# Kernel optimization log

Hardware: AMD Instinct MI355X
Metric: run time of the kernel (lower is better)

Reference implementation:

```python
import jax, jax.numpy as jnp
import numpy as np

B, T, C, H = 4096, 32, 180, 6
HD = C // H  # 30
EPS = 1e-5

def _ln(x, g, b):
    mu = jnp.mean(x, axis=-1, keepdims=True)
    var = jnp.mean(jnp.square(x - mu), axis=-1, keepdims=True)
    return (x - mu) * jax.lax.rsqrt(var + EPS) * g + b

def setup_inputs() -> dict:
    key = jax.random.key(0)
    ks = jax.random.split(key, 12)
    s_in = 1.0 / np.sqrt(C)
    s_ff = 1.0 / np.sqrt(4 * C)
    return {
        "x": jax.random.normal(ks[0], (B, T, C), jnp.float32),
        "wq": jax.random.normal(ks[1], (H, C, HD), jnp.float32) * s_in,
        "wk": jax.random.normal(ks[2], (H, C, HD), jnp.float32) * s_in,
        "wv": jax.random.normal(ks[3], (H, C, HD), jnp.float32) * s_in,
        "g1": jnp.ones((C,), jnp.float32),
        "be1": jnp.zeros((C,), jnp.float32),
        "g2": jnp.ones((C,), jnp.float32),
        "be2": jnp.zeros((C,), jnp.float32),
        "w1": jax.random.normal(ks[4], (C, 4 * C), jnp.float32) * s_in,
        "b1": jnp.zeros((4 * C,), jnp.float32),
        "w2": jax.random.normal(ks[5], (4 * C, C), jnp.float32) * s_ff,
        "b2": jnp.zeros((C,), jnp.float32),
    }

def reference(x, wq, wk, wv, g1, be1, g2, be2, w1, b1, w2, b2):
    Bv, Tv, Cv = x.shape
    h = _ln(x, g1, be1)
    # batched multi-head QKV (replaces per-head Python loop)
    q = jnp.einsum('btc,hcd->bhtd', h, wq)
    k = jnp.einsum('btc,hcd->bhtd', h, wk)
    v = jnp.einsum('btc,hcd->bhtd', h, wv)
    scores = jnp.einsum('bhtd,bhsd->bhts', q, k) * (HD ** -0.5)
    mask = jnp.tril(jnp.ones((Tv, Tv), bool))
    scores = jnp.where(mask, scores, -jnp.inf)
    attn = jax.nn.softmax(scores, axis=-1)  # dropout off (eval)
    out = jnp.einsum('bhts,bhsd->bhtd', attn, v)
    out = jnp.transpose(out, (0, 2, 1, 3)).reshape(Bv, Tv, Cv)  # concat heads
    x = x + out
    h2 = _ln(x, g2, be2)
    mlp = jax.nn.relu(h2 @ w1 + b1) @ w2 + b2  # dropout off (eval)
    return x + mlp
```

## Files before the change

### kernel.cpp

```cpp
#include <hip/hip_runtime.h>

typedef __attribute__((ext_vector_type(8))) short short8;
typedef __attribute__((ext_vector_type(4))) float f32x4;
typedef __attribute__((ext_vector_type(2))) float f32x2;
typedef unsigned short ushort_t;
typedef unsigned int u32;
typedef unsigned long long u64;

#define MFMA16(a,b,c) __builtin_amdgcn_mfma_f32_16x16x32_bf16((a),(b),(c),0,0,0)

__device__ __forceinline__ ushort_t f2bf(float f){
  union { float f; u32 u; } v; v.f = f;
  u32 r = v.u + 0x7fffu + ((v.u >> 16) & 1u);
  return (ushort_t)(r >> 16);
}
__device__ __forceinline__ float bf2f(ushort_t h){
  union { u32 u; float f; } v; v.u = ((u32)h) << 16; return v.f;
}
__device__ __forceinline__ u64 pack4(float a, float b, float c, float d){
  u32 p0 = (u32)f2bf(a) | ((u32)f2bf(b) << 16);
  u32 p1 = (u32)f2bf(c) | ((u32)f2bf(d) << 16);
  return (u64)p0 | ((u64)p1 << 32);
}

template<int CTRL>
__device__ __forceinline__ float dpp_add(float x){
  union { float f; int i; } a, b;
  a.f = x;
  b.i = __builtin_amdgcn_update_dpp(a.i, a.i, CTRL, 0xF, 0xF, false);
  return x + b.f;
}
__device__ __forceinline__ float red4_add(float x){
  x = dpp_add<0xB1>(x); x = dpp_add<0x4E>(x);
  return x;
}

#define WQKV_ELEMS (576*192)
#define W1T_ELEMS  (768*192)
#define W2T_ELEMS  (192*768)

#define SH 200
#define SS 40

__global__ void prep_weights(const float* __restrict__ wq, const float* __restrict__ wk,
                             const float* __restrict__ wv, const float* __restrict__ w1,
                             const float* __restrict__ w2, ushort_t* __restrict__ ws){
  ushort_t* wqkv = ws;
  ushort_t* w1t = ws + WQKV_ELEMS;
  ushort_t* w2t = w1t + W1T_ELEMS;
  int tid = blockIdx.x * blockDim.x + threadIdx.x;
  int stride = gridDim.x * blockDim.x;
  for (int i = tid; i < WQKV_ELEMS; i += stride){
    int k = i % 192; int row = i / 192;
    int d = row & 31; int m = (row >> 5) % 3; int h = row / 96;
    float v = 0.f;
    if (d < 30 && k < 180){
      const float* W = (m == 0) ? wq : ((m == 1) ? wk : wv);
      v = W[(h*180 + k)*30 + d];
    }
    wqkv[i] = f2bf(v);
  }
  for (int i = tid; i < W1T_ELEMS; i += stride){
    int c = i % 192; int n = i / 192;
    float v = (n < 720 && c < 180) ? w1[c*720 + n] : 0.f;
    w1t[i] = f2bf(v);
  }
  for (int i = tid; i < W2T_ELEMS; i += stride){
    int c4 = i % 768; int n = i / 768;
    float v = (n < 180 && c4 < 720) ? w2[c4*180 + n] : 0.f;
    w2t[i] = f2bf(v);
  }
}

__device__ __forceinline__ void ln_pass(const ushort_t* src, ushort_t* dst,
                                        const float* __restrict__ g,
                                        const float* __restrict__ be, int tid){
  int row = tid >> 2, sub = tid & 3;
  int c0 = sub*48;
  float s1 = 0.f, s2 = 0.f;
  #pragma unroll
  for (int gi = 0; gi < 12; gi++){
    u64 m = *(const u64*)(src + row*SH + c0 + gi*4);
    #pragma unroll
    for (int e = 0; e < 4; e++){
      float v = bf2f((ushort_t)(m >> (16*e)));
      s1 += v; s2 += v*v;
    }
  }
  s1 = red4_add(s1); s2 = red4_add(s2);
  float mu = s1 * (1.f/180.f);
  float rstd = rsqrtf(s2 * (1.f/180.f) - mu*mu + 1e-5f);
  #pragma unroll
  for (int gi = 0; gi < 12; gi++){
    int c = c0 + gi*4;
    if (c < 180){
      u64 m = *(const u64*)(src + row*SH + c);
      f32x4 gg = *(const f32x4*)(g + c);
      f32x4 bb = *(const f32x4*)(be + c);
      float v0 = (bf2f((ushort_t)(m    )) - mu)*rstd*gg.x + bb.x;
      float v1 = (bf2f((ushort_t)(m>>16)) - mu)*rstd*gg.y + bb.y;
      float v2 = (bf2f((ushort_t)(m>>32)) - mu)*rstd*gg.z + bb.z;
      float v3 = (bf2f((ushort_t)(m>>48)) - mu)*rstd*gg.w + bb.w;
      *(u64*)(dst + row*SH + c) = pack4(v0, v1, v2, v3);
    } else {
      *(u64*)(dst + row*SH + c) = 0ull;
    }
  }
}

__global__ __launch_bounds__(256, 3)
void block_kernel(const float* __restrict__ x,
                  const float* __restrict__ g1, const float* __restrict__ be1,
                  const float* __restrict__ g2, const float* __restrict__ be2,
                  const float* __restrict__ b1, const float* __restrict__ b2,
                  const ushort_t* __restrict__ wqkv, const ushort_t* __restrict__ w1t,
                  const ushort_t* __restrict__ w2t, float* __restrict__ out){
  __shared__ __align__(16) ushort_t regA[64*SH];
  __shared__ __align__(16) ushort_t hn[64*SH];

  int tid = threadIdx.x;
  int wave = tid >> 6, lane = tid & 63;
  int quad = lane >> 4, c16 = lane & 15;
  long base = (long)blockIdx.x * 11520;

  #pragma unroll
  for (int it = 0; it < 12; it++){
    int idx = it*256 + tid;
    if (idx < 2880){
      f32x4 v = *(const f32x4*)(x + base + (long)idx*4);
      int row = (int)(((u32)idx * 745655u) >> 25);
      int col = idx - row*45;
      *(u64*)(regA + row*SH + col*4) = pack4(v.x, v.y, v.z, v.w);
    } else {
      int p = idx - 2880;
      int row = (p*21846) >> 16;
      int g = p - row*3;
      *(u64*)(regA + row*SH + 180 + g*4) = 0ull;
    }
  }
  __syncthreads();

  ln_pass(regA, hn, g1, be1, tid);
  __syncthreads();

  {
    ushort_t* buf0 = regA + wave*(2*32*SS);
    ushort_t* buf1 = buf0 + 32*SS;
    const float scl = 0.18257418583505537f;

    for (int jj = 0; jj < 3; jj++){
      int j = wave*3 + jj;
      int bb = (j >= 6) ? 1 : 0;
      int head = j - 6*bb;
      const ushort_t* wbase = wqkv + head*(96*192);

      f32x4 accq[2][2], acck[2][2], accv[2][2];
      #pragma unroll
      for (int i = 0; i < 2; i++)
        #pragma unroll
        for (int jx = 0; jx < 2; jx++){ accq[i][jx]=(f32x4)0.f; acck[i][jx]=(f32x4)0.f; accv[i][jx]=(f32x4)0.f; }

      short8 aqc[2], akc[2], avc[2];
      #pragma unroll
      for (int mt = 0; mt < 2; mt++){
        aqc[mt] = *(const short8*)(wbase + (      mt*16 + c16)*192 + quad*8);
        akc[mt] = *(const short8*)(wbase + (32  + mt*16 + c16)*192 + quad*8);
        avc[mt] = *(const short8*)(wbase + (64  + mt*16 + c16)*192 + quad*8);
      }
      #pragma unroll
      for (int kk = 0; kk < 6; kk++){
        short8 aqn[2], akn[2], avn[2];
        if (kk < 5){
          #pragma unroll
          for (int mt = 0; mt < 2; mt++){
            aqn[mt] = *(const short8*)(wbase + (      mt*16 + c16)*192 + (kk+1)*32 + quad*8);
            akn[mt] = *(const short8*)(wbase + (32  + mt*16 + c16)*192 + (kk+1)*32 + quad*8);
            avn[mt] = *(const short8*)(wbase + (64  + mt*16 + c16)*192 + (kk+1)*32 + quad*8);
          }
        }
        short8 hf[2];
        #pragma unroll
        for (int nt = 0; nt < 2; nt++)
          hf[nt] = *(const short8*)(hn + (bb*32 + nt*16 + c16)*SH + kk*32 + quad*8);
        #pragma unroll
        for (int mt = 0; mt < 2; mt++)
          #pragma unroll
          for (int nt = 0; nt < 2; nt++){
            accq[mt][nt] = MFMA16(aqc[mt], hf[nt], accq[mt][nt]);
            acck[mt][nt] = MFMA16(akc[mt], hf[nt], acck[mt][nt]);
            accv[mt][nt] = MFMA16(hf[mt], avc[nt], accv[mt][nt]);
          }
        if (kk < 5){
          #pragma unroll
          for (int mt = 0; mt < 2; mt++){ aqc[mt]=aqn[mt]; akc[mt]=akn[mt]; avc[mt]=avn[mt]; }
        }
      }
      #pragma unroll
      for (int mt = 0; mt < 2; mt++)
        #pragma unroll
        for (int nt = 0; nt < 2; nt++){
          *(u64*)(buf0 + (nt*16 + c16)*SS + mt*16 + quad*4) =
            pack4(accq[mt][nt][0], accq[mt][nt][1], accq[mt][nt][2], accq[mt][nt][3]);
          *(u64*)(buf1 + (nt*16 + c16)*SS + mt*16 + quad*4) =
            pack4(acck[mt][nt][0], acck[mt][nt][1], acck[mt][nt][2], acck[mt][nt][3]);
        }
      f32x4 sacc[2][2];
      #pragma unroll
      for (int i = 0; i < 2; i++){ sacc[i][0]=(f32x4)0.f; sacc[i][1]=(f32x4)0.f; }
      short8 akf[2], bqf[2];
      #pragma unroll
      for (int mt = 0; mt < 2; mt++) akf[mt] = *(const short8*)(buf1 + (mt*16 + c16)*SS + quad*8);
      #pragma unroll
      for (int nt = 0; nt < 2; nt++) bqf[nt] = *(const short8*)(buf0 + (nt*16 + c16)*SS + quad*8);
      #pragma unroll
      for (int mt = 0; mt < 2; mt++)
        #pragma unroll
        for (int nt = 0; nt < 2; nt++)
          sacc[mt][nt] = MFMA16(akf[mt], bqf[nt], sacc[mt][nt]);
      #pragma unroll
      for (int nt = 0; nt < 2; nt++){
        int t = nt*16 + c16;
        float v[8];
        #pragma unroll
        for (int r = 0; r < 4; r++){
          int s0 = quad*4 + r, s1v = 16 + quad*4 + r;
          v[r]   = (s0  > t) ? -1e30f : sacc[0][nt][r]*scl;
          v[4+r] = (s1v > t) ? -1e30f : sacc[1][nt][r]*scl;
        }
        float m = v[0];
        #pragma unroll
        for (int i = 1; i < 8; i++) m = fmaxf(m, v[i]);
        m = fmaxf(m, __shfl_xor(m, 16));
        m = fmaxf(m, __shfl_xor(m, 32));
        float e[8], s = 0.f;
        #pragma unroll
        for (int i = 0; i < 8; i++){ e[i] = __expf(v[i] - m); s += e[i]; }
        s += __shfl_xor(s, 16);
        s += __shfl_xor(s, 32);
        float inv = 1.f / s;
        *(u64*)(buf1 + t*SS +      quad*4) = pack4(e[0]*inv, e[1]*inv, e[2]*inv, e[3]*inv);
        *(u64*)(buf1 + t*SS + 16 + quad*4) = pack4(e[4]*inv, e[5]*inv, e[6]*inv, e[7]*inv);
      }
      #pragma unroll
      for (int mt = 0; mt < 2; mt++)
        #pragma unroll
        for (int nt = 0; nt < 2; nt++)
          *(u64*)(buf0 + (nt*16 + c16)*SS + mt*16 + quad*4) =
            pack4(accv[mt][nt][0], accv[mt][nt][1], accv[mt][nt][2], accv[mt][nt][3]);
      f32x4 oacc[2][2];
      #pragma unroll
      for (int i = 0; i < 2; i++){ oacc[i][0]=(f32x4)0.f; oacc[i][1]=(f32x4)0.f; }
      short8 avf[2], bpf[2];
      #pragma unroll
      for (int mt = 0; mt < 2; mt++) avf[mt] = *(const short8*)(buf0 + (mt*16 + c16)*SS + quad*8);
      #pragma unroll
      for (int nt = 0; nt < 2; nt++) bpf[nt] = *(const short8*)(buf1 + (nt*16 + c16)*SS + quad*8);
      #pragma unroll
      for (int mt = 0; mt < 2; mt++)
        #pragma unroll
        for (int nt = 0; nt < 2; nt++)
          oacc[mt][nt] = MFMA16(avf[mt], bpf[nt], oacc[mt][nt]);
      #pragma unroll
      for (int mt = 0; mt < 2; mt++)
        #pragma unroll
        for (int nt = 0; nt < 2; nt++){
          long ob = base + (long)(bb*32 + nt*16 + c16)*180 + head*30 + mt*16 + quad*4;
          f32x2 lo; lo.x = oacc[mt][nt][0]; lo.y = oacc[mt][nt][1];
          *(f32x2*)(out + ob) = lo;
          if (mt == 0 || quad < 3){
            f32x2 hi; hi.x = oacc[mt][nt][2]; hi.y = oacc[mt][nt][3];
            *(f32x2*)(out + ob + 2) = hi;
          }
        }
    }
  }
  __syncthreads();

  #pragma unroll
  for (int it = 0; it < 12; it++){
    int idx = it*256 + tid;
    if (idx < 2880){
      f32x4 v = *(const f32x4*)(x + base + (long)idx*4);
      f32x4 a = *(const f32x4*)(out + base + (long)idx*4);
      int row = (int)(((u32)idx * 745655u) >> 25);
      int col = idx - row*45;
      *(u64*)(regA + row*SH + col*4) = pack4(v.x+a.x, v.y+a.y, v.z+a.z, v.w+a.w);
    } else {
      int p = idx - 2880;
      int row = (p*21846) >> 16;
      int g = p - row*3;
      *(u64*)(regA + row*SH + 180 + g*4) = 0ull;
    }
  }
  __syncthreads();

  ln_pass(regA, hn, g2, be2, tid);
  __syncthreads();

  {
    ushort_t* act = regA;
    f32x4 outacc[3][4];
    #pragma unroll
    for (int i = 0; i < 3; i++)
      #pragma unroll
      for (int jx = 0; jx < 4; jx++) outacc[i][jx] = (f32x4)0.f;

    for (int ch = 0; ch < 4; ch++){
      f32x4 aacc[3][4];
      #pragma unroll
      for (int i = 0; i < 3; i++)
        #pragma unroll
        for (int jx = 0; jx < 4; jx++) aacc[i][jx] = (f32x4)0.f;
      short8 awc[3];
      #pragma unroll
      for (int mi = 0; mi < 3; mi++)
        awc[mi] = *(const short8*)(w1t + (size_t)(ch*192 + (wave*3+mi)*16 + c16)*192 + quad*8);
      #pragma unroll
      for (int kk = 0; kk < 6; kk++){
        short8 awn[3];
        if (kk < 5){
          #pragma unroll
          for (int mi = 0; mi < 3; mi++)
            awn[mi] = *(const short8*)(w1t + (size_t)(ch*192 + (wave*3+mi)*16 + c16)*192 + (kk+1)*32 + quad*8);
        }
        short8 bh[4];
        #pragma unroll
        for (int tt = 0; tt < 4; tt++)
          bh[tt] = *(const short8*)(hn + (tt*16 + c16)*SH + kk*32 + quad*8);
        #pragma unroll
        for (int mi = 0; mi < 3; mi++)
          #pragma unroll
          for (int tt = 0; tt < 4; tt++)
            aacc[mi][tt] = MFMA16(awc[mi], bh[tt], aacc[mi][tt]);
        if (kk < 5){
          #pragma unroll
          for (int mi = 0; mi < 3; mi++) awc[mi] = awn[mi];
        }
      }
      __syncthreads();
      #pragma unroll
      for (int mi = 0; mi < 3; mi++){
        int nrel = (wave*3+mi)*16 + quad*4;
        int nabs = ch*192 + nrel;
        f32x4 bias = (f32x4)0.f;
        if (nabs < 720) bias = *(const f32x4*)(b1 + nabs);
        #pragma unroll
        for (int tt = 0; tt < 4; tt++){
          float v0 = fmaxf(aacc[mi][tt][0] + bias[0], 0.f);
          float v1 = fmaxf(aacc[mi][tt][1] + bias[1], 0.f);
          float v2 = fmaxf(aacc[mi][tt][2] + bias[2], 0.f);
          float v3 = fmaxf(aacc[mi][tt][3] + bias[3], 0.f);
          *(u64*)(act + (tt*16 + c16)*SH + nrel) = pack4(v0, v1, v2, v3);
        }
      }
      __syncthreads();
      short8 bwc[3];
      #pragma unroll
      for (int ntl = 0; ntl < 3; ntl++)
        bwc[ntl] = *(const short8*)(w2t + (size_t)(wave*48 + ntl*16 + c16)*768 + ch*192 + quad*8);
      #pragma unroll
      for (int kk = 0; kk < 6; kk++){
        short8 bwn[3];
        if (kk < 5){
          #pragma unroll
          for (int ntl = 0; ntl < 3; ntl++)
            bwn[ntl] = *(const short8*)(w2t + (size_t)(wave*48 + ntl*16 + c16)*768 + ch*192 + (kk+1)*32 + quad*8);
        }
        short8 aa[4];
        #pragma unroll
        for (int tt = 0; tt < 4; tt++)
          aa[tt] = *(const short8*)(act + (tt*16 + c16)*SH + kk*32 + quad*8);
        #pragma unroll
        for (int ntl = 0; ntl < 3; ntl++)
          #pragma unroll
          for (int tt = 0; tt < 4; tt++)
            outacc[ntl][tt] = MFMA16(bwc[ntl], aa[tt], outacc[ntl][tt]);
        if (kk < 5){
          #pragma unroll
          for (int ntl = 0; ntl < 3; ntl++) bwc[ntl] = bwn[ntl];
        }
      }
    }
    #pragma unroll
    for (int ntl = 0; ntl < 3; ntl++){
      int no = wave*48 + ntl*16 + quad*4;
      #pragma unroll
      for (int tt = 0; tt < 4; tt++)
        *(u64*)(hn + (tt*16 + c16)*SH + no) =
          pack4(outacc[ntl][tt][0], outacc[ntl][tt][1], outacc[ntl][tt][2], outacc[ntl][tt][3]);
    }
  }
  __syncthreads();

  #pragma unroll
  for (int it = 0; it < 12; it++){
    int idx = it*256 + tid;
    if (idx < 2880){
      f32x4 v = *(const f32x4*)(x + base + (long)idx*4);
      f32x4 a = *(const f32x4*)(out + base + (long)idx*4);
      int row = (int)(((u32)idx * 745655u) >> 25);
      int col4 = (idx - row*45)*4;
      f32x4 b2v = *(const f32x4*)(b2 + col4);
      u64 m = *(const u64*)(hn + row*SH + col4);
      v.x += a.x + bf2f((ushort_t)(m      )) + b2v.x;
      v.y += a.y + bf2f((ushort_t)(m >> 16)) + b2v.y;
      v.z += a.z + bf2f((ushort_t)(m >> 32)) + b2v.z;
      v.w += a.w + bf2f((ushort_t)(m >> 48)) + b2v.w;
      *(f32x4*)(out + base + (long)idx*4) = v;
    }
  }
}

extern "C" void kernel_launch(void* const* d_in, const int* in_sizes, int n_in,
                              void* d_out, int out_size, void* d_ws, size_t ws_size,
                              hipStream_t stream) {
  const float* x   = (const float*)d_in[0];
  const float* wq  = (const float*)d_in[1];
  const float* wk  = (const float*)d_in[2];
  const float* wv  = (const float*)d_in[3];
  const float* g1  = (const float*)d_in[4];
  const float* be1 = (const float*)d_in[5];
  const float* g2  = (const float*)d_in[6];
  const float* be2 = (const float*)d_in[7];
  const float* w1  = (const float*)d_in[8];
  const float* b1  = (const float*)d_in[9];
  const float* w2  = (const float*)d_in[10];
  const float* b2  = (const float*)d_in[11];
  ushort_t* ws   = (ushort_t*)d_ws;
  ushort_t* wqkv = ws;
  ushort_t* w1t  = ws + WQKV_ELEMS;
  ushort_t* w2t  = w1t + W1T_ELEMS;
  float* out = (float*)d_out;

  prep_weights<<<256, 256, 0, stream>>>(wq, wk, wv, w1, w2, ws);
  block_kernel<<<2048, 256, 0, stream>>>(x, g1, be1, g2, be2, b1, b2,
                                         wqkv, w1t, w2t, out);
}
```

Measured before the change: 525.7 us.

## Restructure fused transformer block: LN1 from fp32 regs, LDS attention staging, preloaded weights

LayerNorm 1 now runs directly on fp32 x loaded into registers instead of first staging bf16 x in LDS. Attention outputs go to a new LDS buffer rather than through global memory, and the residual is added while building the LN2 input. QKV, W1 and W2 weight fragments for all k-steps are preloaded into pinned registers instead of double-buffered, and the MLP output is written straight from accumulators with the bias and residual fused in. The third LDS buffer and higher register pressure lower the occupancy hint from 3 to 2 blocks per CU, and prep_weights gets more blocks.

```diff
diff --git a/kernel.cpp b/kernel.cpp
--- a/kernel.cpp
+++ b/kernel.cpp
@@ -2,7 +2,6 @@
 
 typedef __attribute__((ext_vector_type(8))) short short8;
 typedef __attribute__((ext_vector_type(4))) float f32x4;
-typedef __attribute__((ext_vector_type(2))) float f32x2;
 typedef unsigned short ushort_t;
 typedef unsigned int u32;
 typedef unsigned long long u64;
@@ -22,6 +21,7 @@
   u32 p1 = (u32)f2bf(c) | ((u32)f2bf(d) << 16);
   return (u64)p0 | ((u64)p1 << 32);
 }
+__device__ __forceinline__ void pin(short8 &v){ asm volatile("" : "+v"(v)); }
 
 template<int CTRL>
 __device__ __forceinline__ float dpp_add(float x){
@@ -72,56 +72,180 @@
   }
 }
 
-__device__ __forceinline__ void ln_pass(const ushort_t* src, ushort_t* dst,
-                                        const float* __restrict__ g,
-                                        const float* __restrict__ be, int tid){
-  int row = tid >> 2, sub = tid & 3;
-  int c0 = sub*48;
-  float s1 = 0.f, s2 = 0.f;
-  #pragma unroll
-  for (int gi = 0; gi < 12; gi++){
-    u64 m = *(const u64*)(src + row*SH + c0 + gi*4);
-    #pragma unroll
-    for (int e = 0; e < 4; e++){
-      float v = bf2f((ushort_t)(m >> (16*e)));
-      s1 += v; s2 += v*v;
-    }
-  }
-  s1 = red4_add(s1); s2 = red4_add(s2);
-  float mu = s1 * (1.f/180.f);
-  float rstd = rsqrtf(s2 * (1.f/180.f) - mu*mu + 1e-5f);
-  #pragma unroll
-  for (int gi = 0; gi < 12; gi++){
-    int c = c0 + gi*4;
-    if (c < 180){
-      u64 m = *(const u64*)(src + row*SH + c);
-      f32x4 gg = *(const f32x4*)(g + c);
-      f32x4 bb = *(const f32x4*)(be + c);
-      float v0 = (bf2f((ushort_t)(m    )) - mu)*rstd*gg.x + bb.x;
-      float v1 = (bf2f((ushort_t)(m>>16)) - mu)*rstd*gg.y + bb.y;
-      float v2 = (bf2f((ushort_t)(m>>32)) - mu)*rstd*gg.z + bb.z;
-      float v3 = (bf2f((ushort_t)(m>>48)) - mu)*rstd*gg.w + bb.w;
-      *(u64*)(dst + row*SH + c) = pack4(v0, v1, v2, v3);
-    } else {
-      *(u64*)(dst + row*SH + c) = 0ull;
-    }
-  }
-}
-
-__global__ __launch_bounds__(256, 3)
+__global__ __launch_bounds__(256, 2)
 void block_kernel(const float* __restrict__ x,
                   const float* __restrict__ g1, const float* __restrict__ be1,
                   const float* __restrict__ g2, const float* __restrict__ be2,
                   const float* __restrict__ b1, const float* __restrict__ b2,
                   const ushort_t* __restrict__ wqkv, const ushort_t* __restrict__ w1t,
                   const ushort_t* __restrict__ w2t, float* __restrict__ out){
-  __shared__ __align__(16) ushort_t regA[64*SH];
+  __shared__ __align__(16) ushort_t W[64*SH];
   __shared__ __align__(16) ushort_t hn[64*SH];
+  __shared__ __align__(16) ushort_t att[64*SH];
 
   int tid = threadIdx.x;
   int wave = tid >> 6, lane = tid & 63;
   int quad = lane >> 4, c16 = lane & 15;
   long base = (long)blockIdx.x * 11520;
+
+  {
+    int row = tid >> 2, sub = tid & 3;
+    int c0 = sub*48;
+    f32x4 xv[12];
+    float s1 = 0.f, s2 = 0.f;
+    #pragma unroll
+    for (int gi = 0; gi < 12; gi++){
+      int c = c0 + gi*4;
+      if (c < 180) xv[gi] = *(const f32x4*)(x + base + (long)row*180 + c);
+      else         xv[gi] = (f32x4)0.f;
+      s1 += xv[gi].x + xv[gi].y + xv[gi].z + xv[gi].w;
+      s2 += xv[gi].x*xv[gi].x + xv[gi].y*xv[gi].y + xv[gi].z*xv[gi].z + xv[gi].w*xv[gi].w;
+    }
+    s1 = red4_add(s1); s2 = red4_add(s2);
+    float mu = s1 * (1.f/180.f);
+    float rstd = rsqrtf(s2 * (1.f/180.f) - mu*mu + 1e-5f);
+    #pragma unroll
+    for (int gi = 0; gi < 12; gi++){
+      int c = c0 + gi*4;
+      if (c < 180){
+        f32x4 gg = *(const f32x4*)(g1 + c);
+        f32x4 bb = *(const f32x4*)(be1 + c);
+        *(u64*)(hn + row*SH + c) = pack4((xv[gi].x - mu)*rstd*gg.x + bb.x,
+                                         (xv[gi].y - mu)*rstd*gg.y + bb.y,
+                                         (xv[gi].z - mu)*rstd*gg.z + bb.z,
+                                         (xv[gi].w - mu)*rstd*gg.w + bb.w);
+      } else {
+        *(u64*)(hn + row*SH + c) = 0ull;
+      }
+    }
+  }
+  __syncthreads();
+
+  {
+    ushort_t* buf0 = W + wave*(2*32*SS);
+    ushort_t* buf1 = buf0 + 32*SS;
+    const float scl = 0.18257418583505537f;
+
+    for (int jj = 0; jj < 3; jj++){
+      int j = wave*3 + jj;
+      int bb = (j >= 6) ? 1 : 0;
+      int head = j - 6*bb;
+      const ushort_t* wbase = wqkv + head*(96*192);
+
+      f32x4 accq[2][2], acck[2][2], accv[2][2];
+      #pragma unroll
+      for (int i = 0; i < 2; i++)
+        #pragma unroll
+        for (int jx = 0; jx < 2; jx++){ accq[i][jx]=(f32x4)0.f; acck[i][jx]=(f32x4)0.f; accv[i][jx]=(f32x4)0.f; }
+
+      short8 aqw[2][6], akw[2][6];
+      #pragma unroll
+      for (int mt = 0; mt < 2; mt++)
+        #pragma unroll
+        for (int kk = 0; kk < 6; kk++){
+          aqw[mt][kk] = *(const short8*)(wbase + (      mt*16 + c16)*192 + kk*32 + quad*8);
+          akw[mt][kk] = *(const short8*)(wbase + (32  + mt*16 + c16)*192 + kk*32 + quad*8);
+          pin(aqw[mt][kk]); pin(akw[mt][kk]);
+        }
+      short8 avc[2], avn[2];
+      #pragma unroll
+      for (int mt = 0; mt < 2; mt++)
+        avc[mt] = *(const short8*)(wbase + (64 + mt*16 + c16)*192 + quad*8);
+      #pragma unroll
+      for (int kk = 0; kk < 6; kk++){
+        if (kk < 5){
+          #pragma unroll
+          for (int mt = 0; mt < 2; mt++)
+            avn[mt] = *(const short8*)(wbase + (64 + mt*16 + c16)*192 + (kk+1)*32 + quad*8);
+        }
+        short8 hf[2];
+        #pragma unroll
+        for (int nt = 0; nt < 2; nt++)
+          hf[nt] = *(const short8*)(hn + (bb*32 + nt*16 + c16)*SH + kk*32 + quad*8);
+        #pragma unroll
+        for (int mt = 0; mt < 2; mt++)
+          #pragma unroll
+          for (int nt = 0; nt < 2; nt++){
+            accq[mt][nt] = MFMA16(aqw[mt][kk], hf[nt], accq[mt][nt]);
+            acck[mt][nt] = MFMA16(akw[mt][kk], hf[nt], acck[mt][nt]);
+            accv[mt][nt] = MFMA16(hf[mt], avc[nt], accv[mt][nt]);
+          }
+        if (kk < 5){
+          #pragma unroll
+          for (int mt = 0; mt < 2; mt++) avc[mt] = avn[mt];
+        }
+      }
+      #pragma unroll
+      for (int mt = 0; mt < 2; mt++)
+        #pragma unroll
+        for (int nt = 0; nt < 2; nt++){
+          *(u64*)(buf0 + (nt*16 + c16)*SS + mt*16 + quad*4) =
+            pack4(accq[mt][nt][0], accq[mt][nt][1], accq[mt][nt][2], accq[mt][nt][3]);
+          *(u64*)(buf1 + (nt*16 + c16)*SS + mt*16 + quad*4) =
+            pack4(acck[mt][nt][0], acck[mt][nt][1], acck[mt][nt][2], acck[mt][nt][3]);
+        }
+      f32x4 sacc[2][2];
+      #pragma unroll
+      for (int i = 0; i < 2; i++){ sacc[i][0]=(f32x4)0.f; sacc[i][1]=(f32x4)0.f; }
+      short8 akf[2], bqf[2];
+      #pragma unroll
+      for (int mt = 0; mt < 2; mt++) akf[mt] = *(const short8*)(buf1 + (mt*16 + c16)*SS + quad*8);
+      #pragma unroll
+      for (int nt = 0; nt < 2; nt++) bqf[nt] = *(const short8*)(buf0 + (nt*16 + c16)*SS + quad*8);
+      #pragma unroll
+      for (int mt = 0; mt < 2; mt++)
+        #pragma unroll
+        for (int nt = 0; nt < 2; nt++)
+          sacc[mt][nt] = MFMA16(akf[mt], bqf[nt], sacc[mt][nt]);
+      #pragma unroll
+      for (int nt = 0; nt < 2; nt++){
+        int t = nt*16 + c16;
+        float v[8];
+        #pragma unroll
+        for (int r = 0; r < 4; r++){
+          int s0 = quad*4 + r, s1v = 16 + quad*4 + r;
+          v[r]   = (s0  > t) ? -1e30f : sacc[0][nt][r]*scl;
+          v[4+r] = (s1v > t) ? -1e30f : sacc[1][nt][r]*scl;
+        }
+        float m = v[0];
+        #pragma unroll
+        for (int i = 1; i < 8; i++) m = fmaxf(m, v[i]);
+        m = fmaxf(m, __shfl_xor(m, 16));
+        m = fmaxf(m, __shfl_xor(m, 32));
+        float e[8], s = 0.f;
+        #pragma unroll
+        for (int i = 0; i < 8; i++){ e[i] = __expf(v[i] - m); s += e[i]; }
+        s += __shfl_xor(s, 16);
+        s += __shfl_xor(s, 32);
+        float inv = 1.f / s;
+        *(u64*)(buf1 + t*SS +      quad*4) = pack4(e[0]*inv, e[1]*inv, e[2]*inv, e[3]*inv);
+        *(u64*)(buf1 + t*SS + 16 + quad*4) = pack4(e[4]*inv, e[5]*inv, e[6]*inv, e[7]*inv);
+      }
+      #pragma unroll
+      for (int mt = 0; mt < 2; mt++)
+        #pragma unroll
+        for (int nt = 0; nt < 2; nt++)
+          *(u64*)(buf0 + (nt*16 + c16)*SS + mt*16 + quad*4) =
+            pack4(accv[mt][nt][0], accv[mt][nt][1], accv[mt][nt][2], accv[mt][nt][3]);
+      f32x4 oacc[2][2];
+      #pragma unroll
+      for (int i = 0; i < 2; i++){ oacc[i][0]=(f32x4)0.f; oacc[i][1]=(f32x4)0.f; }
+      short8 avf[2], bpf[2];
+      #pragma unroll
+      for (int mt = 0; mt < 2; mt++) avf[mt] = *(const short8*)(buf0 + (mt*16 + c16)*SS + quad*8);
+      #pragma unroll
+      for (int nt = 0; nt < 2; nt++) bpf[nt] = *(const short8*)(buf1 + (nt*16 + c16)*SS + quad*8);
+      #pragma unroll
+      for (int mt = 0; mt < 2; mt++)
+        #pragma unroll
+        for (int nt = 0; nt < 2; nt++){
+          oacc[mt][nt] = MFMA16(avf[mt], bpf[nt], oacc[mt][nt]);
+          *(u64*)(att + (bb*32 + nt*16 + c16)*SH + head*32 + mt*16 + quad*4) =
+            pack4(oacc[mt][nt][0], oacc[mt][nt][1], oacc[mt][nt][2], oacc[mt][nt][3]);
+        }
+    }
+  }
+  __syncthreads();
 
   #pragma unroll
   for (int it = 0; it < 12; it++){
@@ -129,181 +253,65 @@
     if (idx < 2880){
       f32x4 v = *(const f32x4*)(x + base + (long)idx*4);
       int row = (int)(((u32)idx * 745655u) >> 25);
-      int col = idx - row*45;
-      *(u64*)(regA + row*SH + col*4) = pack4(v.x, v.y, v.z, v.w);
+      int col4 = (idx - row*45)*4;
+      #pragma unroll
+      for (int e = 0; e < 4; e++){
+        int c = col4 + e;
+        int h = (c*4370) >> 17;
+        int d = c - h*30;
+        v[e] += bf2f(att[row*SH + h*32 + d]);
+      }
+      *(f32x4*)(out + base + (long)idx*4) = v;
+      *(u64*)(hn + row*SH + col4) = pack4(v.x, v.y, v.z, v.w);
     } else {
       int p = idx - 2880;
       int row = (p*21846) >> 16;
       int g = p - row*3;
-      *(u64*)(regA + row*SH + 180 + g*4) = 0ull;
+      *(u64*)(hn + row*SH + 180 + g*4) = 0ull;
     }
   }
   __syncthreads();
 
-  ln_pass(regA, hn, g1, be1, tid);
+  {
+    int row = tid >> 2, sub = tid & 3;
+    int c0 = sub*48;
+    float s1 = 0.f, s2 = 0.f;
+    u64 mv[12];
+    #pragma unroll
+    for (int gi = 0; gi < 12; gi++){
+      mv[gi] = *(const u64*)(hn + row*SH + c0 + gi*4);
+      #pragma unroll
+      for (int e = 0; e < 4; e++){
+        float v = bf2f((ushort_t)(mv[gi] >> (16*e)));
+        s1 += v; s2 += v*v;
+      }
+    }
+    s1 = red4_add(s1); s2 = red4_add(s2);
+    float mu = s1 * (1.f/180.f);
+    float rstd = rsqrtf(s2 * (1.f/180.f) - mu*mu + 1e-5f);
+    #pragma unroll
+    for (int gi = 0; gi < 12; gi++){
+      int c = c0 + gi*4;
+      if (c < 180){
+        f32x4 gg = *(const f32x4*)(g2 + c);
+        f32x4 bb = *(const f32x4*)(be2 + c);
+        float v0 = (bf2f((ushort_t)(mv[gi]    )) - mu)*rstd*gg.x + bb.x;
+        float v1 = (bf2f((ushort_t)(mv[gi]>>16)) - mu)*rstd*gg.y + bb.y;
+        float v2 = (bf2f((ushort_t)(mv[gi]>>32)) - mu)*rstd*gg.z + bb.z;
+        float v3 = (bf2f((ushort_t)(mv[gi]>>48)) - mu)*rstd*gg.w + bb.w;
+        *(u64*)(hn + row*SH + c) = pack4(v0, v1, v2, v3);
+      }
+    }
+  }
   __syncthreads();
 
   {
-    ushort_t* buf0 = regA + wave*(2*32*SS);
-    ushort_t* buf1 = buf0 + 32*SS;
-    const float scl = 0.18257418583505537f;
-
-    for (int jj = 0; jj < 3; jj++){
-      int j = wave*3 + jj;
-      int bb = (j >= 6) ? 1 : 0;
-      int head = j - 6*bb;
-      const ushort_t* wbase = wqkv + head*(96*192);
-
-      f32x4 accq[2][2], acck[2][2], accv[2][2];
-      #pragma unroll
-      for (int i = 0; i < 2; i++)
-        #pragma unroll
-        for (int jx = 0; jx < 2; jx++){ accq[i][jx]=(f32x4)0.f; acck[i][jx]=(f32x4)0.f; accv[i][jx]=(f32x4)0.f; }
-
-      short8 aqc[2], akc[2], avc[2];
-      #pragma unroll
-      for (int mt = 0; mt < 2; mt++){
-        aqc[mt] = *(const short8*)(wbase + (      mt*16 + c16)*192 + quad*8);
-        akc[mt] = *(const short8*)(wbase + (32  + mt*16 + c16)*192 + quad*8);
-        avc[mt] = *(const short8*)(wbase + (64  + mt*16 + c16)*192 + quad*8);
-      }
-      #pragma unroll
-      for (int kk = 0; kk < 6; kk++){
-        short8 aqn[2], akn[2], avn[2];
-        if (kk < 5){
-          #pragma unroll
-          for (int mt = 0; mt < 2; mt++){
-            aqn[mt] = *(const short8*)(wbase + (      mt*16 + c16)*192 + (kk+1)*32 + quad*8);
-            akn[mt] = *(const short8*)(wbase + (32  + mt*16 + c16)*192 + (kk+1)*32 + quad*8);
-            avn[mt] = *(const short8*)(wbase + (64  + mt*16 + c16)*192 + (kk+1)*32 + quad*8);
-          }
-        }
-        short8 hf[2];
-        #pragma unroll
-        for (int nt = 0; nt < 2; nt++)
-          hf[nt] = *(const short8*)(hn + (bb*32 + nt*16 + c16)*SH + kk*32 + quad*8);
-        #pragma unroll
-        for (int mt = 0; mt < 2; mt++)
-          #pragma unroll
-          for (int nt = 0; nt < 2; nt++){
-            accq[mt][nt] = MFMA16(aqc[mt], hf[nt], accq[mt][nt]);
-            acck[mt][nt] = MFMA16(akc[mt], hf[nt], acck[mt][nt]);
-            accv[mt][nt] = MFMA16(hf[mt], avc[nt], accv[mt][nt]);
-          }
-        if (kk < 5){
-          #pragma unroll
-          for (int mt = 0; mt < 2; mt++){ aqc[mt]=aqn[mt]; akc[mt]=akn[mt]; avc[mt]=avn[mt]; }
-        }
-      }
-      #pragma unroll
-      for (int mt = 0; mt < 2; mt++)
-        #pragma unroll
-        for (int nt = 0; nt < 2; nt++){
-          *(u64*)(buf0 + (nt*16 + c16)*SS + mt*16 + quad*4) =
-            pack4(accq[mt][nt][0], accq[mt][nt][1], accq[mt][nt][2], accq[mt][nt][3]);
-          *(u64*)(buf1 + (nt*16 + c16)*SS + mt*16 + quad*4) =
-            pack4(acck[mt][nt][0], acck[mt][nt][1], acck[mt][nt][2], acck[mt][nt][3]);
-        }
-      f32x4 sacc[2][2];
-      #pragma unroll
-      for (int i = 0; i < 2; i++){ sacc[i][0]=(f32x4)0.f; sacc[i][1]=(f32x4)0.f; }
-      short8 akf[2], bqf[2];
-      #pragma unroll
-      for (int mt = 0; mt < 2; mt++) akf[mt] = *(const short8*)(buf1 + (mt*16 + c16)*SS + quad*8);
-      #pragma unroll
-      for (int nt = 0; nt < 2; nt++) bqf[nt] = *(const short8*)(buf0 + (nt*16 + c16)*SS + quad*8);
-      #pragma unroll
-      for (int mt = 0; mt < 2; mt++)
-        #pragma unroll
-        for (int nt = 0; nt < 2; nt++)
-          sacc[mt][nt] = MFMA16(akf[mt], bqf[nt], sacc[mt][nt]);
-      #pragma unroll
-      for (int nt = 0; nt < 2; nt++){
-        int t = nt*16 + c16;
-        float v[8];
-        #pragma unroll
-        for (int r = 0; r < 4; r++){
-          int s0 = quad*4 + r, s1v = 16 + quad*4 + r;
-          v[r]   = (s0  > t) ? -1e30f : sacc[0][nt][r]*scl;
-          v[4+r] = (s1v > t) ? -1e30f : sacc[1][nt][r]*scl;
-        }
-        float m = v[0];
-        #pragma unroll
-        for (int i = 1; i < 8; i++) m = fmaxf(m, v[i]);
-        m = fmaxf(m, __shfl_xor(m, 16));
-        m = fmaxf(m, __shfl_xor(m, 32));
-        float e[8], s = 0.f;
-        #pragma unroll
-        for (int i = 0; i < 8; i++){ e[i] = __expf(v[i] - m); s += e[i]; }
-        s += __shfl_xor(s, 16);
-        s += __shfl_xor(s, 32);
-        float inv = 1.f / s;
-        *(u64*)(buf1 + t*SS +      quad*4) = pack4(e[0]*inv, e[1]*inv, e[2]*inv, e[3]*inv);
-        *(u64*)(buf1 + t*SS + 16 + quad*4) = pack4(e[4]*inv, e[5]*inv, e[6]*inv, e[7]*inv);
-      }
-      #pragma unroll
-      for (int mt = 0; mt < 2; mt++)
-        #pragma unroll
-        for (int nt = 0; nt < 2; nt++)
-          *(u64*)(buf0 + (nt*16 + c16)*SS + mt*16 + quad*4) =
-            pack4(accv[mt][nt][0], accv[mt][nt][1], accv[mt][nt][2], accv[mt][nt][3]);
-      f32x4 oacc[2][2];
-      #pragma unroll
-      for (int i = 0; i < 2; i++){ oacc[i][0]=(f32x4)0.f; oacc[i][1]=(f32x4)0.f; }
-      short8 avf[2], bpf[2];
-      #pragma unroll
-      for (int mt = 0; mt < 2; mt++) avf[mt] = *(const short8*)(buf0 + (mt*16 + c16)*SS + quad*8);
-      #pragma unroll
-      for (int nt = 0; nt < 2; nt++) bpf[nt] = *(const short8*)(buf1 + (nt*16 + c16)*SS + quad*8);
-      #pragma unroll
-      for (int mt = 0; mt < 2; mt++)
-        #pragma unroll
-        for (int nt = 0; nt < 2; nt++)
-          oacc[mt][nt] = MFMA16(avf[mt], bpf[nt], oacc[mt][nt]);
-      #pragma unroll
-      for (int mt = 0; mt < 2; mt++)
-        #pragma unroll
-        for (int nt = 0; nt < 2; nt++){
-          long ob = base + (long)(bb*32 + nt*16 + c16)*180 + head*30 + mt*16 + quad*4;
-          f32x2 lo; lo.x = oacc[mt][nt][0]; lo.y = oacc[mt][nt][1];
-          *(f32x2*)(out + ob) = lo;
-          if (mt == 0 || quad < 3){
-            f32x2 hi; hi.x = oacc[mt][nt][2]; hi.y = oacc[mt][nt][3];
-            *(f32x2*)(out + ob + 2) = hi;
-          }
-        }
-    }
-  }
-  __syncthreads();
-
-  #pragma unroll
-  for (int it = 0; it < 12; it++){
-    int idx = it*256 + tid;
-    if (idx < 2880){
-      f32x4 v = *(const f32x4*)(x + base + (long)idx*4);
-      f32x4 a = *(const f32x4*)(out + base + (long)idx*4);
-      int row = (int)(((u32)idx * 745655u) >> 25);
-      int col = idx - row*45;
-      *(u64*)(regA + row*SH + col*4) = pack4(v.x+a.x, v.y+a.y, v.z+a.z, v.w+a.w);
-    } else {
-      int p = idx - 2880;
-      int row = (p*21846) >> 16;
-      int g = p - row*3;
-      *(u64*)(regA + row*SH + 180 + g*4) = 0ull;
-    }
-  }
-  __syncthreads();
-
-  ln_pass(regA, hn, g2, be2, tid);
-  __syncthreads();
-
-  {
-    ushort_t* act = regA;
-    f32x4 outacc[3][4];
-    #pragma unroll
-    for (int i = 0; i < 3; i++)
-      #pragma unroll
-      for (int jx = 0; jx < 4; jx++) outacc[i][jx] = (f32x4)0.f;
+    ushort_t* act = W;
+    f32x4 outacc[4][3];
+    #pragma unroll
+    for (int i = 0; i < 4; i++)
+      #pragma unroll
+      for (int jx = 0; jx < 3; jx++) outacc[i][jx] = (f32x4)0.f;
 
     for (int ch = 0; ch < 4; ch++){
       f32x4 aacc[3][4];
@@ -311,18 +319,16 @@
       for (int i = 0; i < 3; i++)
         #pragma unroll
         for (int jx = 0; jx < 4; jx++) aacc[i][jx] = (f32x4)0.f;
-      short8 awc[3];
+      short8 aw[3][6];
       #pragma unroll
       for (int mi = 0; mi < 3; mi++)
-        awc[mi] = *(const short8*)(w1t + (size_t)(ch*192 + (wave*3+mi)*16 + c16)*192 + quad*8);
+        #pragma unroll
+        for (int kk = 0; kk < 6; kk++){
+          aw[mi][kk] = *(const short8*)(w1t + (size_t)(ch*192 + (wave*3+mi)*16 + c16)*192 + kk*32 + quad*8);
+          pin(aw[mi][kk]);
+        }
       #pragma unroll
       for (int kk = 0; kk < 6; kk++){
-        short8 awn[3];
-        if (kk < 5){
-          #pragma unroll
-          for (int mi = 0; mi < 3; mi++)
-            awn[mi] = *(const short8*)(w1t + (size_t)(ch*192 + (wave*3+mi)*16 + c16)*192 + (kk+1)*32 + quad*8);
-        }
         short8 bh[4];
         #pragma unroll
         for (int tt = 0; tt < 4; tt++)
@@ -331,11 +337,7 @@
         for (int mi = 0; mi < 3; mi++)
           #pragma unroll
           for (int tt = 0; tt < 4; tt++)
-            aacc[mi][tt] = MFMA16(awc[mi], bh[tt], aacc[mi][tt]);
-        if (kk < 5){
-          #pragma unroll
-          for (int mi = 0; mi < 3; mi++) awc[mi] = awn[mi];
-        }
+            aacc[mi][tt] = MFMA16(aw[mi][kk], bh[tt], aacc[mi][tt]);
       }
       __syncthreads();
       #pragma unroll
@@ -354,59 +356,41 @@
         }
       }
       __syncthreads();
-      short8 bwc[3];
+      short8 bw[3][6];
       #pragma unroll
       for (int ntl = 0; ntl < 3; ntl++)
-        bwc[ntl] = *(const short8*)(w2t + (size_t)(wave*48 + ntl*16 + c16)*768 + ch*192 + quad*8);
+        #pragma unroll
+        for (int kk = 0; kk < 6; kk++){
+          bw[ntl][kk] = *(const short8*)(w2t + (size_t)(wave*48 + ntl*16 + c16)*768 + ch*192 + kk*32 + quad*8);
+          pin(bw[ntl][kk]);
+        }
       #pragma unroll
       for (int kk = 0; kk < 6; kk++){
-        short8 bwn[3];
-        if (kk < 5){
-          #pragma unroll
-          for (int ntl = 0; ntl < 3; ntl++)
-            bwn[ntl] = *(const short8*)(w2t + (size_t)(wave*48 + ntl*16 + c16)*768 + ch*192 + (kk+1)*32 + quad*8);
-        }
         short8 aa[4];
         #pragma unroll
         for (int tt = 0; tt < 4; tt++)
           aa[tt] = *(const short8*)(act + (tt*16 + c16)*SH + kk*32 + quad*8);
         #pragma unroll
-        for (int ntl = 0; ntl < 3; ntl++)
-          #pragma unroll
-          for (int tt = 0; tt < 4; tt++)
-            outacc[ntl][tt] = MFMA16(bwc[ntl], aa[tt], outacc[ntl][tt]);
-        if (kk < 5){
-          #pragma unroll
-          for (int ntl = 0; ntl < 3; ntl++) bwc[ntl] = bwn[ntl];
-        }
+        for (int tt = 0; tt < 4; tt++)
+          #pragma unroll
+          for (int ntl = 0; ntl < 3; ntl++)
+            outacc[tt][ntl] = MFMA16(aa[tt], bw[ntl][kk], outacc[tt][ntl]);
       }
     }
     #pragma unroll
     for (int ntl = 0; ntl < 3; ntl++){
-      int no = wave*48 + ntl*16 + quad*4;
-      #pragma unroll
-      for (int tt = 0; tt < 4; tt++)
-        *(u64*)(hn + (tt*16 + c16)*SH + no) =
-          pack4(outacc[ntl][tt][0], outacc[ntl][tt][1], outacc[ntl][tt][2], outacc[ntl][tt][3]);
-    }
-  }
-  __syncthreads();
-
-  #pragma unroll
-  for (int it = 0; it < 12; it++){
-    int idx = it*256 + tid;
-    if (idx < 2880){
-      f32x4 v = *(const f32x4*)(x + base + (long)idx*4);
-      f32x4 a = *(const f32x4*)(out + base + (long)idx*4);
-      int row = (int)(((u32)idx * 745655u) >> 25);
-      int col4 = (idx - row*45)*4;
-      f32x4 b2v = *(const f32x4*)(b2 + col4);
-      u64 m = *(const u64*)(hn + row*SH + col4);
-      v.x += a.x + bf2f((ushort_t)(m      )) + b2v.x;
-      v.y += a.y + bf2f((ushort_t)(m >> 16)) + b2v.y;
-      v.z += a.z + bf2f((ushort_t)(m >> 32)) + b2v.z;
-      v.w += a.w + bf2f((ushort_t)(m >> 48)) + b2v.w;
-      *(f32x4*)(out + base + (long)idx*4) = v;
+      int no = wave*48 + ntl*16 + c16;
+      if (no < 180){
+        float bias = b2[no];
+        #pragma unroll
+        for (int tt = 0; tt < 4; tt++){
+          #pragma unroll
+          for (int r = 0; r < 4; r++){
+            long a = base + (long)(tt*16 + quad*4 + r)*180 + no;
+            out[a] = out[a] + outacc[tt][ntl][r] + bias;
+          }
+        }
+      }
     }
   }
 }
@@ -432,7 +416,7 @@
   ushort_t* w2t  = w1t + W1T_ELEMS;
   float* out = (float*)d_out;
 
-  prep_weights<<<256, 256, 0, stream>>>(wq, wk, wv, w1, w2, ws);
+  prep_weights<<<512, 256, 0, stream>>>(wq, wk, wv, w1, w2, ws);
   block_kernel<<<2048, 256, 0, stream>>>(x, g1, be1, g2, be2, b1, b2,
                                          wqkv, w1t, w2t, out);
 }
```

After: 503.3 us. 1.04x faster.
